# Kernel tuning notes

Hardware: AMD Instinct MI355X
Metric: run time of the kernel (lower is better)

## Reference

```python
import jax, jax.numpy as jnp
import numpy as np

N, D, H, O, E, K = 4096, 512, 1024, 512, 8, 2


def setup_inputs() -> dict:
    key = jax.random.key(0)
    ks = jax.random.split(key, 7)
    s = 0.02
    return {
        "x": jax.random.normal(ks[0], (N, D), dtype=jnp.float32),
        "W1": jax.random.normal(ks[1], (E, D, H), dtype=jnp.float32) * s,
        "b1": jnp.zeros((E, H), dtype=jnp.float32),
        "W2": jax.random.normal(ks[2], (E, H, O), dtype=jnp.float32) * s,
        "b2": jnp.zeros((E, O), dtype=jnp.float32),
        "Wg": jax.random.normal(ks[3], (D, E), dtype=jnp.float32) * s,
        "bg": jnp.zeros((E,), dtype=jnp.float32),
        "k": K,
    }


def reference(x, W1, b1, W2, b2, Wg, bg, k):
    # Gating: softmax over experts, then top-k with renormalized weights
    gates = jax.nn.softmax(x @ Wg + bg, axis=1)              # [N, E]
    topv, topi = jax.lax.top_k(gates, k)                     # [N, k]
    w = topv / jnp.sum(topv, axis=1, keepdims=True)          # renormalized top-k weights

    # Dense per-expert two-layer MLP (grouped GEMM form)
    h = jax.nn.relu(jnp.einsum('nd,edh->neh', x, W1) + b1[None])   # [N, E, H]
    y = jnp.einsum('neh,eho->neo', h, W2) + b2[None]               # [N, E, O]

    # Gather selected experts and combine
    y_sel = jnp.take_along_axis(y, topi[:, :, None], axis=1)       # [N, k, O]
    out = jnp.einsum('nko,nk->no', y_sel, w)                       # [N, O]
    return out, gates, topi
```

## Files before the change

### kernel.cpp

```cpp
#include <hip/hip_runtime.h>
#include <hip/hip_bf16.h>

#define N_TOK 4096
#define DIM   512
#define HID   1024
#define OUTD  512
#define NEXP  8
#define TOPK  2

#define MT1 72
#define HROWS 9216

typedef __bf16 bf16;
typedef bf16  bf16x8 __attribute__((ext_vector_type(8)));
typedef bf16  bf16x4 __attribute__((ext_vector_type(4)));
typedef float f32x4  __attribute__((ext_vector_type(4)));

__device__ inline f32x4 mfma16(bf16x8 a, bf16x8 b, f32x4 c) {
    return __builtin_amdgcn_mfma_f32_16x16x32_bf16(a, b, c, 0, 0, 0);
}

__device__ inline void gload16(const bf16* g, char* l) {
    __builtin_amdgcn_global_load_lds(
        (const __attribute__((address_space(1))) void*)g,
        (__attribute__((address_space(3))) void*)l, 16, 0, 0);
}

__device__ inline void find_tile(const int* cv, int mt, int& e, int& rb, int& i0, int& ce)
{
    int at = 0, base = 0;
    e = 0; rb = 0; i0 = 0; ce = 0;
#pragma unroll
    for (int ee = 0; ee < NEXP; ++ee) {
        int c = cv[ee]; int n1 = (c + 127) >> 7;
        if (mt >= at && mt < at + n1) {
            e = ee; int lt = mt - at; rb = base + lt * 128; i0 = lt * 128; ce = c;
        }
        at += n1; base += n1 << 7;
    }
}

__device__ inline int tiles_total(const int* cv)
{
    int t = 0;
#pragma unroll
    for (int ee = 0; ee < NEXP; ++ee) t += (cv[ee] + 127) >> 7;
    return t;
}

__global__ __launch_bounds__(256) void prep_gate_kernel(
    const float* __restrict__ W1, const float* __restrict__ W2,
    const float* __restrict__ Wg, const float* __restrict__ bg,
    const float* __restrict__ x,
    bf16* __restrict__ W1t, bf16* __restrict__ W2t,
    bf16* __restrict__ xb,
    float* __restrict__ gates_out, float* __restrict__ topi_out,
    int* __restrict__ pick_e, float* __restrict__ pick_w)
{
    __shared__ __align__(16) float smem[NEXP * DIM];
    int b = blockIdx.x;

    if (b >= 8192) {
        const float4* Wg4 = (const float4*)Wg;
        for (int i = threadIdx.x; i < DIM * NEXP / 4; i += 256) {
            float4 v = Wg4[i];
#pragma unroll
            for (int j = 0; j < 4; ++j) {
                int idx = i * 4 + j;
                smem[(idx & 7) * DIM + (idx >> 3)] = ((const float*)&v)[j];
            }
        }
        __syncthreads();

        int wave = threadIdx.x >> 6;
        int lane = threadIdx.x & 63;
        int n = (b - 8192) * 4 + wave;

        const float4* x4 = (const float4*)(x + (size_t)n * DIM);
        float4 v0 = x4[lane];
        float4 v1 = x4[lane + 64];

        bf16x4 o0 = { (bf16)v0.x, (bf16)v0.y, (bf16)v0.z, (bf16)v0.w };
        bf16x4 o1 = { (bf16)v1.x, (bf16)v1.y, (bf16)v1.z, (bf16)v1.w };
        bf16x4* xb4 = (bf16x4*)(xb + (size_t)n * DIM);
        xb4[lane]      = o0;
        xb4[lane + 64] = o1;

        float acc[NEXP];
#pragma unroll
        for (int e = 0; e < NEXP; ++e) {
            const float4* wr = (const float4*)(smem + e * DIM);
            float4 w0 = wr[lane];
            float4 w1 = wr[lane + 64];
            acc[e] = v0.x * w0.x + v0.y * w0.y + v0.z * w0.z + v0.w * w0.w
                   + v1.x * w1.x + v1.y * w1.y + v1.z * w1.z + v1.w * w1.w;
        }
#pragma unroll
        for (int off = 32; off >= 1; off >>= 1) {
#pragma unroll
            for (int e = 0; e < NEXP; ++e) acc[e] += __shfl_xor(acc[e], off, 64);
        }
#pragma unroll
        for (int e = 0; e < NEXP; ++e) acc[e] += bg[e];

        float m = acc[0];
#pragma unroll
        for (int e = 1; e < NEXP; ++e) m = fmaxf(m, acc[e]);
        float g[NEXP];
        float s = 0.f;
#pragma unroll
        for (int e = 0; e < NEXP; ++e) { g[e] = expf(acc[e] - m); s += g[e]; }
        float inv_s = 1.f / s;
#pragma unroll
        for (int e = 0; e < NEXP; ++e) g[e] *= inv_s;

        if (lane < NEXP) gates_out[n * NEXP + lane] = g[lane];

        if (lane == 0) {
            int m1 = 0;
#pragma unroll
            for (int e = 1; e < NEXP; ++e) if (g[e] > g[m1]) m1 = e;
            int m2 = (m1 == 0) ? 1 : 0;
#pragma unroll
            for (int e = 0; e < NEXP; ++e) if (e != m1 && g[e] > g[m2]) m2 = e;
            float v1g = g[m1], v2g = g[m2];
            float inv = 1.f / (v1g + v2g);
            topi_out[n * TOPK + 0] = (float)m1;
            topi_out[n * TOPK + 1] = (float)m2;
            int2 pe = { m1, m2 };
            float2 pw = { v1g * inv, v2g * inv };
            *(int2*)(pick_e + n * 2) = pe;
            *(float2*)(pick_w + n * 2) = pw;
        }
        return;
    }

    float (*tile)[33] = (float(*)[33])smem;
    const float* src; bf16* dst; int R, C, tilex, rem, e;
    if (b < 4096) {
        e = b >> 9; rem = b & 511; R = DIM; C = HID; tilex = 32;
        src = W1; dst = W1t;
    } else {
        b -= 4096;
        e = b >> 9; rem = b & 511; R = HID; C = OUTD; tilex = 16;
        src = W2; dst = W2t;
    }
    const float* s = src + (size_t)e * R * C;
    bf16* d = dst + (size_t)e * R * C;
    int c0 = (rem % tilex) * 32, r0 = (rem / tilex) * 32;

    int tx = threadIdx.x & 31, ty = threadIdx.x >> 5;
#pragma unroll
    for (int i = 0; i < 4; ++i) {
        int r = ty + i * 8;
        tile[r][tx] = s[(size_t)(r0 + r) * C + c0 + tx];
    }
    __syncthreads();

    int t = threadIdx.x;
    int dc = t >> 3, q = t & 7;
    bf16x4 v;
#pragma unroll
    for (int j = 0; j < 4; ++j) v[j] = (bf16)tile[q * 4 + j][dc];
    *(bf16x4*)(d + (size_t)(c0 + dc) * R + r0 + q * 4) = v;
}

__global__ __launch_bounds__(256) void bucket_kernel(
    const int* __restrict__ pick_e,
    int* __restrict__ counts, int* __restrict__ tlist)
{
    __shared__ int cnt;
    if (threadIdx.x == 0) cnt = 0;
    __syncthreads();
    int e = blockIdx.x;
    for (int i = threadIdx.x; i < N_TOK * 2; i += 256) {
        if (pick_e[i] == e) {
            int p = atomicAdd(&cnt, 1);
            tlist[e * N_TOK + p] = i;
        }
    }
    __syncthreads();
    if (threadIdx.x == 0) counts[e] = cnt;
}


__global__ __launch_bounds__(256, 4) void l1_kernel(
    const bf16* __restrict__ xb, const bf16* __restrict__ W1t,
    const float* __restrict__ b1, const int* __restrict__ counts,
    const int* __restrict__ tlist, bf16* __restrict__ h)
{
    int cv[NEXP];
#pragma unroll
    for (int e = 0; e < NEXP; ++e) cv[e] = counts[e];
    if (blockIdx.x >= tiles_total(cv) * 8) return;
    int mt = blockIdx.x >> 3, nt = blockIdx.x & 7;
    int e, rb, i0, cnt;
    find_tile(cv, mt, e, rb, i0, cnt);

    __shared__ __align__(16) char lds[32768];

    int tid = threadIdx.x, w = tid >> 6, l = tid & 63;
    int c0 = w * 128 + l, c1 = c0 + 64;
    int rA0 = c0 >> 2, rA1 = c1 >> 2;
    int kA0 = (c0 & 3) ^ ((rA0 & 3) ^ ((rA0 >> 2) & 1));
    int kA1 = (c1 & 3) ^ ((rA1 & 3) ^ ((rA1 >> 2) & 1));
    int iA0 = i0 + rA0, iA1 = i0 + rA1;
    const int* tl = tlist + e * N_TOK;
    int tok0 = iA0 < cnt ? (tl[iA0] >> 1) : 0;
    int tok1 = iA1 < cnt ? (tl[iA1] >> 1) : 0;
    const bf16* sA0 = xb + (size_t)tok0 * DIM + kA0 * 8;
    const bf16* sA1 = xb + (size_t)tok1 * DIM + kA1 * 8;
    int n0 = nt * 128;
    const bf16* w1e = W1t + (size_t)e * HID * DIM;
    const bf16* sB0 = w1e + (size_t)(n0 + rA0) * DIM + kA0 * 8;
    const bf16* sB1 = w1e + (size_t)(n0 + rA1) * DIM + kA1 * 8;
    int oA0 = c0 * 16, oA1 = c1 * 16;

    f32x4 acc[4][4];
#pragma unroll
    for (int mf = 0; mf < 4; ++mf)
#pragma unroll
        for (int nf = 0; nf < 4; ++nf) acc[mf][nf] = (f32x4){0.f, 0.f, 0.f, 0.f};

    int wm = w >> 1, wn = w & 1;
    int lr = l & 15;
    int kb = ((l >> 4) ^ ((l & 3) ^ ((l >> 2) & 1))) * 16;

    {
        char* A = lds;       char* B = lds + 8192;
        gload16(sA0, A + oA0); gload16(sA1, A + oA1);
        gload16(sB0, B + oA0); gload16(sB1, B + oA1);
    }

    for (int ks = 0; ks < 16; ++ks) {
        __syncthreads();
        if (ks < 15) {
            char* A = lds + (((ks + 1) & 1) * 16384);
            char* B = A + 8192;
            int kof = (ks + 1) * 32;
            gload16(sA0 + kof, A + oA0); gload16(sA1 + kof, A + oA1);
            gload16(sB0 + kof, B + oA0); gload16(sB1 + kof, B + oA1);
        }
        char* A = lds + ((ks & 1) * 16384);
        char* B = A + 8192;
        bf16x8 af[4], bfr[4];
#pragma unroll
        for (int mf = 0; mf < 4; ++mf)
            af[mf] = *(const bf16x8*)(A + (wm * 64 + mf * 16 + lr) * 64 + kb);
#pragma unroll
        for (int nf = 0; nf < 4; ++nf)
            bfr[nf] = *(const bf16x8*)(B + (wn * 64 + nf * 16 + lr) * 64 + kb);
#pragma unroll
        for (int mf = 0; mf < 4; ++mf)
#pragma unroll
            for (int nf = 0; nf < 4; ++nf)
                acc[mf][nf] = mfma16(af[mf], bfr[nf], acc[mf][nf]);
    }

    const float* b1e = b1 + e * HID;
#pragma unroll
    for (int nf = 0; nf < 4; ++nf) {
        int colg = n0 + wn * 64 + nf * 16 + lr;
        float bias = b1e[colg];
#pragma unroll
        for (int mf = 0; mf < 4; ++mf) {
#pragma unroll
            for (int r = 0; r < 4; ++r) {
                int gr = rb + wm * 64 + mf * 16 + (l >> 4) * 4 + r;
                float v = fmaxf(acc[mf][nf][r] + bias, 0.f);
                h[(size_t)gr * HID + colg] = (bf16)v;
            }
        }
    }
}

__global__ __launch_bounds__(256, 4) void l2_kernel(
    const bf16* __restrict__ h, const bf16* __restrict__ W2t,
    const int* __restrict__ counts, const int* __restrict__ tlist,
    bf16* __restrict__ ybuf)
{
    int cv[NEXP];
#pragma unroll
    for (int e = 0; e < NEXP; ++e) cv[e] = counts[e];
    if (blockIdx.x >= tiles_total(cv) * 8) return;
    int mth = blockIdx.x >> 2, nt = blockIdx.x & 3;
    int mt = mth >> 1, half = mth & 1;
    int e, rb, i0, cnt;
    find_tile(cv, mt, e, rb, i0, cnt);
    rb += half * 64; i0 += half * 64;

    __shared__ __align__(16) char lds[24576];

    int tid = threadIdx.x, w = tid >> 6, l = tid & 63;
    int cA = tid; int rA = cA >> 2;
    int kA = (cA & 3) ^ ((rA & 3) ^ ((rA >> 2) & 1));
    const bf16* sA = h + (size_t)(rb + rA) * HID + kA * 8;
    int cB0 = w * 128 + l, cB1 = cB0 + 64;
    int rB0 = cB0 >> 2, rB1 = cB1 >> 2;
    int kB0 = (cB0 & 3) ^ ((rB0 & 3) ^ ((rB0 >> 2) & 1));
    int kB1 = (cB1 & 3) ^ ((rB1 & 3) ^ ((rB1 >> 2) & 1));
    int n0 = nt * 128;
    const bf16* w2e = W2t + (size_t)e * OUTD * HID;
    const bf16* sB0 = w2e + (size_t)(n0 + rB0) * HID + kB0 * 8;
    const bf16* sB1 = w2e + (size_t)(n0 + rB1) * HID + kB1 * 8;
    int oA = cA * 16, oB0 = cB0 * 16, oB1 = cB1 * 16;

    f32x4 acc[2][4];
#pragma unroll
    for (int mf = 0; mf < 2; ++mf)
#pragma unroll
        for (int nf = 0; nf < 4; ++nf) acc[mf][nf] = (f32x4){0.f, 0.f, 0.f, 0.f};

    int wm = w >> 1, wn = w & 1;
    int lr = l & 15;
    int kb = ((l >> 4) ^ ((l & 3) ^ ((l >> 2) & 1))) * 16;

    {
        char* A = lds; char* B = lds + 4096;
        gload16(sA, A + oA); gload16(sB0, B + oB0); gload16(sB1, B + oB1);
    }

    for (int ks = 0; ks < 32; ++ks) {
        __syncthreads();
        if (ks < 31) {
            char* A = lds + (((ks + 1) & 1) * 12288);
            char* B = A + 4096;
            int kof = (ks + 1) * 32;
            gload16(sA + kof, A + oA);
            gload16(sB0 + kof, B + oB0); gload16(sB1 + kof, B + oB1);
        }
        char* A = lds + ((ks & 1) * 12288);
        char* B = A + 4096;
        bf16x8 af[2], bfr[4];
#pragma unroll
        for (int mf = 0; mf < 2; ++mf)
            af[mf] = *(const bf16x8*)(A + (wm * 32 + mf * 16 + lr) * 64 + kb);
#pragma unroll
        for (int nf = 0; nf < 4; ++nf)
            bfr[nf] = *(const bf16x8*)(B + (wn * 64 + nf * 16 + lr) * 64 + kb);
#pragma unroll
        for (int mf = 0; mf < 2; ++mf)
#pragma unroll
            for (int nf = 0; nf < 4; ++nf)
                acc[mf][nf] = mfma16(af[mf], bfr[nf], acc[mf][nf]);
    }

    const int* tl = tlist + e * N_TOK;
#pragma unroll
    for (int mf = 0; mf < 2; ++mf) {
#pragma unroll
        for (int r = 0; r < 4; ++r) {
            int rloc = wm * 32 + mf * 16 + (l >> 4) * 4 + r;
            int i = i0 + rloc;
            if (i < cnt) {
                int pi = tl[i];
                bf16* yrow = ybuf + (size_t)pi * OUTD;
#pragma unroll
                for (int nf = 0; nf < 4; ++nf)
                    yrow[n0 + wn * 64 + nf * 16 + lr] = (bf16)acc[mf][nf][r];
            }
        }
    }
}

__global__ __launch_bounds__(256) void combine_kernel(
    const bf16* __restrict__ ybuf, const float* __restrict__ b2,
    const int* __restrict__ pick_e, const float* __restrict__ pick_w,
    float* __restrict__ out)
{
    int w = threadIdx.x >> 6;
    int l = threadIdx.x & 63;
#pragma unroll
    for (int j = 0; j < 2; ++j) {
        int n = blockIdx.x * 8 + w * 2 + j;
        int e0 = pick_e[n * 2], e1 = pick_e[n * 2 + 1];
        float w0 = pick_w[n * 2], w1 = pick_w[n * 2 + 1];

        const bf16x8* y0 = (const bf16x8*)(ybuf + (size_t)(n * 2) * OUTD);
        const bf16x8* y1 = (const bf16x8*)(ybuf + (size_t)(n * 2 + 1) * OUTD);
        const float4* b20 = (const float4*)(b2 + e0 * OUTD);
        const float4* b21 = (const float4*)(b2 + e1 * OUTD);
        float4* o4 = (float4*)(out + (size_t)n * OUTD);

        bf16x8 a = y0[l];
        bf16x8 b = y1[l];
        float4 c0 = b20[l * 2], c1 = b20[l * 2 + 1];
        float4 d0 = b21[l * 2], d1 = b21[l * 2 + 1];

        float4 r0, r1;
        r0.x = w0 * ((float)a[0] + c0.x) + w1 * ((float)b[0] + d0.x);
        r0.y = w0 * ((float)a[1] + c0.y) + w1 * ((float)b[1] + d0.y);
        r0.z = w0 * ((float)a[2] + c0.z) + w1 * ((float)b[2] + d0.z);
        r0.w = w0 * ((float)a[3] + c0.w) + w1 * ((float)b[3] + d0.w);
        r1.x = w0 * ((float)a[4] + c1.x) + w1 * ((float)b[4] + d1.x);
        r1.y = w0 * ((float)a[5] + c1.y) + w1 * ((float)b[5] + d1.y);
        r1.z = w0 * ((float)a[6] + c1.z) + w1 * ((float)b[6] + d1.z);
        r1.w = w0 * ((float)a[7] + c1.w) + w1 * ((float)b[7] + d1.w);
        o4[l * 2]     = r0;
        o4[l * 2 + 1] = r1;
    }
}

extern "C" void kernel_launch(void* const* d_in, const int* in_sizes, int n_in,
                              void* d_out, int out_size, void* d_ws, size_t ws_size,
                              hipStream_t stream)
{
    const float* x  = (const float*)d_in[0];
    const float* W1 = (const float*)d_in[1];
    const float* b1 = (const float*)d_in[2];
    const float* W2 = (const float*)d_in[3];
    const float* b2 = (const float*)d_in[4];
    const float* Wg = (const float*)d_in[5];
    const float* bg = (const float*)d_in[6];

    float* out_f   = (float*)d_out;
    float* gates_o = out_f + (size_t)N_TOK * OUTD;
    float* topi_o  = gates_o + (size_t)N_TOK * NEXP;

    char* ws = (char*)d_ws;
    size_t offW1t = 0;
    size_t offW2t = offW1t + (size_t)NEXP * HID * DIM * 2;
    size_t offXb  = offW2t + (size_t)NEXP * OUTD * HID * 2;
    size_t offH   = offXb + (size_t)N_TOK * DIM * 2;
    size_t offYb  = offH + (size_t)HROWS * HID * 2;
    size_t offCnt = offYb + (size_t)N_TOK * 2 * OUTD * 2;
    size_t offTl  = offCnt + 256;
    size_t offPkE = offTl + (size_t)NEXP * N_TOK * 4;
    size_t offPkW = offPkE + (size_t)N_TOK * 2 * 4;

    bf16*  W1t    = (bf16*)(ws + offW1t);
    bf16*  W2t    = (bf16*)(ws + offW2t);
    bf16*  xbuf   = (bf16*)(ws + offXb);
    bf16*  hbuf   = (bf16*)(ws + offH);
    bf16*  ybuf   = (bf16*)(ws + offYb);
    int*   cnts   = (int*)(ws + offCnt);
    int*   tlist  = (int*)(ws + offTl);
    int*   pick_e = (int*)(ws + offPkE);
    float* pick_w = (float*)(ws + offPkW);

    prep_gate_kernel<<<8192 + N_TOK / 4, 256, 0, stream>>>(
        W1, W2, Wg, bg, x, W1t, W2t, xbuf, gates_o, topi_o, pick_e, pick_w);

    bucket_kernel<<<NEXP, 256, 0, stream>>>(pick_e, cnts, tlist);

    l1_kernel<<<MT1 * 8, 256, 0, stream>>>(xbuf, W1t, b1, cnts, tlist, hbuf);
    l2_kernel<<<MT1 * 8, 256, 0, stream>>>(hbuf, W2t, cnts, tlist, ybuf);

    combine_kernel<<<N_TOK / 8, 256, 0, stream>>>(ybuf, b2, pick_e, pick_w, out_f);
}
```

Baseline: 84.40 us.

## Remap GEMM blocks per XCD and enlarge L2 tiles to 128x128

Adds an XCD-aware block-to-work mapping for both grouped GEMM kernels, so consecutive work items, which share expert weights and A rows, land on the same XCD and its L2 cache. The second-layer kernel switches from 64x128 tiles to 128x128 tiles with a 4x4 MFMA fragment per wave, which halves the block count and doubles operand reuse per LDS load. The cost is more accumulator registers and more LDS per block, which may lower occupancy, and fewer blocks to fill the GPU.

Result: faster. 81.70 us (-3.2%).

```diff
diff --git a/kernel.cpp b/kernel.cpp
--- a/kernel.cpp
+++ b/kernel.cpp
@@ -46,6 +46,16 @@
 #pragma unroll
     for (int ee = 0; ee < NEXP; ++ee) t += (cv[ee] + 127) >> 7;
     return t;
+}
+
+__device__ inline int xcd_work_id(int bid, int W)
+{
+    int xcd = bid & 7, idx = bid >> 3;
+    int q = W >> 3, r = W & 7;
+    int start = xcd < r ? xcd * (q + 1) : r * (q + 1) + (xcd - r) * q;
+    int csz   = xcd < r ? q + 1 : q;
+    if (idx >= csz) return -1;
+    return start + idx;
 }
 
 __global__ __launch_bounds__(256) void prep_gate_kernel(
@@ -192,8 +202,9 @@
     int cv[NEXP];
 #pragma unroll
     for (int e = 0; e < NEXP; ++e) cv[e] = counts[e];
-    if (blockIdx.x >= tiles_total(cv) * 8) return;
-    int mt = blockIdx.x >> 3, nt = blockIdx.x & 7;
+    int wid = xcd_work_id(blockIdx.x, tiles_total(cv) * 8);
+    if (wid < 0) return;
+    int mt = wid >> 3, nt = wid & 7;
     int e, rb, i0, cnt;
     find_tile(cv, mt, e, rb, i0, cnt);
 
@@ -282,32 +293,30 @@
     int cv[NEXP];
 #pragma unroll
     for (int e = 0; e < NEXP; ++e) cv[e] = counts[e];
-    if (blockIdx.x >= tiles_total(cv) * 8) return;
-    int mth = blockIdx.x >> 2, nt = blockIdx.x & 3;
-    int mt = mth >> 1, half = mth & 1;
+    int wid = xcd_work_id(blockIdx.x, tiles_total(cv) * 4);
+    if (wid < 0) return;
+    int mt = wid >> 2, nt = wid & 3;
     int e, rb, i0, cnt;
     find_tile(cv, mt, e, rb, i0, cnt);
-    rb += half * 64; i0 += half * 64;
-
-    __shared__ __align__(16) char lds[24576];
+
+    __shared__ __align__(16) char lds[32768];
 
     int tid = threadIdx.x, w = tid >> 6, l = tid & 63;
-    int cA = tid; int rA = cA >> 2;
-    int kA = (cA & 3) ^ ((rA & 3) ^ ((rA >> 2) & 1));
-    const bf16* sA = h + (size_t)(rb + rA) * HID + kA * 8;
-    int cB0 = w * 128 + l, cB1 = cB0 + 64;
-    int rB0 = cB0 >> 2, rB1 = cB1 >> 2;
-    int kB0 = (cB0 & 3) ^ ((rB0 & 3) ^ ((rB0 >> 2) & 1));
-    int kB1 = (cB1 & 3) ^ ((rB1 & 3) ^ ((rB1 >> 2) & 1));
+    int c0 = w * 128 + l, c1 = c0 + 64;
+    int rA0 = c0 >> 2, rA1 = c1 >> 2;
+    int kA0 = (c0 & 3) ^ ((rA0 & 3) ^ ((rA0 >> 2) & 1));
+    int kA1 = (c1 & 3) ^ ((rA1 & 3) ^ ((rA1 >> 2) & 1));
+    const bf16* sA0 = h + (size_t)(rb + rA0) * HID + kA0 * 8;
+    const bf16* sA1 = h + (size_t)(rb + rA1) * HID + kA1 * 8;
     int n0 = nt * 128;
     const bf16* w2e = W2t + (size_t)e * OUTD * HID;
-    const bf16* sB0 = w2e + (size_t)(n0 + rB0) * HID + kB0 * 8;
-    const bf16* sB1 = w2e + (size_t)(n0 + rB1) * HID + kB1 * 8;
-    int oA = cA * 16, oB0 = cB0 * 16, oB1 = cB1 * 16;
-
-    f32x4 acc[2][4];
-#pragma unroll
-    for (int mf = 0; mf < 2; ++mf)
+    const bf16* sB0 = w2e + (size_t)(n0 + rA0) * HID + kA0 * 8;
+    const bf16* sB1 = w2e + (size_t)(n0 + rA1) * HID + kA1 * 8;
+    int oA0 = c0 * 16, oA1 = c1 * 16;
+
+    f32x4 acc[4][4];
+#pragma unroll
+    for (int mf = 0; mf < 4; ++mf)
 #pragma unroll
         for (int nf = 0; nf < 4; ++nf) acc[mf][nf] = (f32x4){0.f, 0.f, 0.f, 0.f};
 
@@ -316,30 +325,31 @@
     int kb = ((l >> 4) ^ ((l & 3) ^ ((l >> 2) & 1))) * 16;
 
     {
-        char* A = lds; char* B = lds + 4096;
-        gload16(sA, A + oA); gload16(sB0, B + oB0); gload16(sB1, B + oB1);
+        char* A = lds;       char* B = lds + 8192;
+        gload16(sA0, A + oA0); gload16(sA1, A + oA1);
+        gload16(sB0, B + oA0); gload16(sB1, B + oA1);
     }
 
     for (int ks = 0; ks < 32; ++ks) {
         __syncthreads();
         if (ks < 31) {
-            char* A = lds + (((ks + 1) & 1) * 12288);
-            char* B = A + 4096;
+            char* A = lds + (((ks + 1) & 1) * 16384);
+            char* B = A + 8192;
             int kof = (ks + 1) * 32;
-            gload16(sA + kof, A + oA);
-            gload16(sB0 + kof, B + oB0); gload16(sB1 + kof, B + oB1);
-        }
-        char* A = lds + ((ks & 1) * 12288);
-        char* B = A + 4096;
-        bf16x8 af[2], bfr[4];
-#pragma unroll
-        for (int mf = 0; mf < 2; ++mf)
-            af[mf] = *(const bf16x8*)(A + (wm * 32 + mf * 16 + lr) * 64 + kb);
+            gload16(sA0 + kof, A + oA0); gload16(sA1 + kof, A + oA1);
+            gload16(sB0 + kof, B + oA0); gload16(sB1 + kof, B + oA1);
+        }
+        char* A = lds + ((ks & 1) * 16384);
+        char* B = A + 8192;
+        bf16x8 af[4], bfr[4];
+#pragma unroll
+        for (int mf = 0; mf < 4; ++mf)
+            af[mf] = *(const bf16x8*)(A + (wm * 64 + mf * 16 + lr) * 64 + kb);
 #pragma unroll
         for (int nf = 0; nf < 4; ++nf)
             bfr[nf] = *(const bf16x8*)(B + (wn * 64 + nf * 16 + lr) * 64 + kb);
 #pragma unroll
-        for (int mf = 0; mf < 2; ++mf)
+        for (int mf = 0; mf < 4; ++mf)
 #pragma unroll
             for (int nf = 0; nf < 4; ++nf)
                 acc[mf][nf] = mfma16(af[mf], bfr[nf], acc[mf][nf]);
@@ -347,10 +357,10 @@
 
     const int* tl = tlist + e * N_TOK;
 #pragma unroll
-    for (int mf = 0; mf < 2; ++mf) {
+    for (int mf = 0; mf < 4; ++mf) {
 #pragma unroll
         for (int r = 0; r < 4; ++r) {
-            int rloc = wm * 32 + mf * 16 + (l >> 4) * 4 + r;
+            int rloc = wm * 64 + mf * 16 + (l >> 4) * 4 + r;
             int i = i0 + rloc;
             if (i < cnt) {
                 int pi = tl[i];
@@ -444,7 +454,7 @@
     bucket_kernel<<<NEXP, 256, 0, stream>>>(pick_e, cnts, tlist);
 
     l1_kernel<<<MT1 * 8, 256, 0, stream>>>(xbuf, W1t, b1, cnts, tlist, hbuf);
-    l2_kernel<<<MT1 * 8, 256, 0, stream>>>(hbuf, W2t, cnts, tlist, ybuf);
+    l2_kernel<<<MT1 * 4, 256, 0, stream>>>(hbuf, W2t, cnts, tlist, ybuf);
 
     combine_kernel<<<N_TOK / 8, 256, 0, stream>>>(ybuf, b2, pick_e, pick_w, out_f);
 }
```
